# Kernel optimization log

Hardware: AMD Instinct MI355X
Metric: run time of the kernel (lower is better)

## Reference

```python
import jax, jax.numpy as jnp
import numpy as np

# Dims: T=64 steps, B=8 batch, H=128 hidden, NH=4 heads, D=2*H=256 cell dim
T, B, H, NH = 64, 8, 128, 4
D = 2 * H
EPS = 1e-5


def _bn(v, scale, bias):
    # flax BatchNorm (training mode): stats over all axes except feature (-1)
    axes = tuple(range(v.ndim - 1))
    mu = v.mean(axes, keepdims=True)
    var = v.var(axes, keepdims=True)
    return (v - mu) * jax.lax.rsqrt(var + EPS) * scale + bias


def setup_inputs() -> dict:
    key = jax.random.key(0)
    ks = iter(jax.random.split(key, 48))
    r = lambda shape, s=0.02: (jax.random.normal(next(ks), shape, jnp.float32) * s)
    z = lambda shape: jnp.zeros(shape, jnp.float32)
    o = lambda shape: jnp.ones(shape, jnp.float32)
    inp = {
        "x": jax.random.normal(next(ks), (T, B, H), jnp.float32),
        # per-head mLSTMCell params (stacked over NH heads), flax Linear: y = x @ W + b
        "Wq": r((NH, D, D)), "bq": z((NH, D)),
        "Wk": r((NH, D, D)), "bk": z((NH, D)),
        "Wv": r((NH, D, D)), "bv": z((NH, D)),
        "conv_k": r((4, 1, NH), 0.2), "conv_b": z((NH,)),  # 1->NH channel conv == per-head 1->1 conv
        "Wi": r((NH, D)), "bi": r((NH,), 0.01),
        "Wf": r((NH, D)),
        "bf": jax.random.uniform(next(ks), (NH,), jnp.float32, 3.0, 6.0),
        "Wo": r((NH, D, D)), "bo": z((NH, D)),
        "Wskip": r((NH, D, D)), "bskip": z((NH, D)),
        # block params
        "bn1_s": o((H,)), "bn1_b": z((H,)),
        "bn2_s": o((D,)), "bn2_b": z((D,)),
        "Wup1": r((H, D)), "bup1": z((D,)),
        "Wup2": r((H, D)), "bup2": z((D,)),
        "Wpoll": r((NH * D, D)), "bpoll": z((D,)),
        "Wdown": r((D, H)), "bdown": z((H,)),
    }
    return inp


def reference(x, Wq, bq, Wk, bk, Wv, bv, conv_k, conv_b, Wi, bi, Wf, bf,
              Wo, bo, Wskip, bskip, bn1_s, bn1_b, bn2_s, bn2_b,
              Wup1, bup1, Wup2, bup2, Wpoll, bpoll, Wdown, bdown):
    nh, d, _ = Wq.shape
    b = x.shape[1]
    inv_sqrt_d = 1.0 / jnp.sqrt(jnp.float32(d))

    def step(carry, xt):
        c, n, m = carry  # c: [nh,b,d,d], n: [nh,b,d], m: [nh,b]
        u = _bn(xt, bn1_s, bn1_b)                      # [b,H]
        trig = jax.nn.silu(u @ Wup2 + bup2)            # [b,d]
        xin = u @ Wup1 + bup1                          # [b,d] mlstm input
        outg = jax.nn.sigmoid(jnp.einsum('bd,hde->hbe', xin, Wo) + bo[:, None, :])
        it = jnp.einsum('bd,hd->hb', xin, Wi) + bi[:, None]
        ft = jnp.einsum('bd,hd->hb', xin, Wf) + bf[:, None]
        m_new = jnp.maximum(ft + m, it)
        ig = jnp.exp(it - m_new)
        fg = jnp.exp(ft + m - m_new)
        # causal-ish depthwise conv over feature axis (flax Conv SAME, k=4)
        qk = jax.lax.conv_general_dilated(xin[..., None], conv_k, (1,), 'SAME',
                                          dimension_numbers=('NWC', 'WIO', 'NWC')) + conv_b
        qk = jax.nn.silu(jnp.transpose(qk, (2, 0, 1)))  # [nh,b,d]
        k = (jnp.einsum('hbd,hde->hbe', qk, Wk) + bk[:, None, :]) * inv_sqrt_d
        q = jnp.einsum('hbd,hde->hbe', qk, Wq) + bq[:, None, :]
        v = jnp.einsum('bd,hde->hbe', xin, Wv) + bv[:, None, :]
        c_new = fg[:, :, None, None] * c + jnp.einsum('hb,hbi,hbj->hbij', ig, v, k)
        n_new = fg[..., None] * n + ig[..., None] * k
        scaler = 1.0 / jnp.maximum(jnp.abs(jnp.einsum('hbi,hbi->hb', n_new, q)), 1.0)
        h = outg * jnp.einsum('hbik,hbk->hbi', c_new, q) * scaler[..., None]
        h = h + jnp.einsum('hbd,hde->hbe', qk, Wskip) + bskip[:, None, :]
        ho = _bn(h, bn2_s, bn2_b)                      # [nh,b,d]
        ho = jnp.transpose(ho, (1, 0, 2)).reshape(b, nh * d)
        ho = ho @ Wpoll + bpoll                        # [b,d]
        y = (ho * trig) @ Wdown + bdown + xt           # residual
        return (c_new, n_new, m_new), y

    c0 = jnp.zeros((nh, b, d, d), x.dtype)
    n0 = jnp.zeros((nh, b, d), x.dtype)
    m0 = jnp.zeros((nh, b), x.dtype)
    _, ys = jax.lax.scan(step, (c0, n0, m0), x)
    return ys
```

## Files before the change

### kernel.cpp

```cpp
#include <hip/hip_runtime.h>
#include <hip/hip_bf16.h>

#define T_ 64
#define B_ 8
#define H_ 128
#define NH_ 4
#define D_ 256
#define TB_ 512
#define EPS_ 1e-5f

typedef short bf16x8 __attribute__((ext_vector_type(8)));
typedef float f32x4 __attribute__((ext_vector_type(4)));

__device__ __forceinline__ float silu_(float x){ return x / (1.0f + __expf(-x)); }
__device__ __forceinline__ float sigm_(float x){ return 1.0f / (1.0f + __expf(-x)); }
__device__ __forceinline__ unsigned short tobf_(float f){
  unsigned u = __float_as_uint(f);
  u += 0x7FFF + ((u >> 16) & 1);
  return (unsigned short)(u >> 16);
}
__device__ __forceinline__ int afrag_(int m, int k){
  return (((m >> 4)*8 + (k >> 5))*64 + ((k >> 3)&3)*16 + (m & 15))*8 + (k & 7);
}
__device__ __forceinline__ int afrag1024_(int m, int k){
  return (((m >> 4)*32 + (k >> 5))*64 + ((k >> 3)&3)*16 + (m & 15))*8 + (k & 7);
}

__device__ __forceinline__ void conv_tile_(const float* __restrict__ Win,
                                           unsigned short* __restrict__ Wout,
                                           int rowstride, int KBS, int tk, int tn,
                                           float (*tl)[132], int tid){
  #pragma unroll
  for (int p = 0; p < 2; p++){
    int r  = p*8 + (tid >> 5);
    int c4 = (tid & 31)*4;
    const float4 v = *(const float4*)(Win + (tk*16 + r)*rowstride + tn*128 + c4);
    tl[r][c4+0] = v.x; tl[r][c4+1] = v.y; tl[r][c4+2] = v.z; tl[r][c4+3] = v.w;
  }
  __syncthreads();
  int nn  = tid >> 5;
  int lqb = (tid >> 4) & 1;
  int lm  = tid & 15;
  int combo = (tn*8 + nn)*KBS + (tk >> 1);
  int l = (2*(tk & 1) + lqb)*16 + lm;
  bf16x8 v;
  #pragma unroll
  for (int j = 0; j < 8; j++) v[j] = (short)tobf_(tl[lqb*8 + j][nn*16 + lm]);
  *(bf16x8*)(Wout + (combo*64 + l)*8) = v;
}

__global__ __launch_bounds__(256) void k_prepup(
    const float* __restrict__ Wq, const float* __restrict__ Wk, const float* __restrict__ Ws,
    const float* __restrict__ Wv, const float* __restrict__ Wo,
    const float* __restrict__ Wup1, const float* __restrict__ Wup2,
    const float* __restrict__ Wp, const float* __restrict__ Wd,
    const float* __restrict__ x, const float* __restrict__ bn1s, const float* __restrict__ bn1b,
    const float* __restrict__ bup1, const float* __restrict__ bup2,
    const float* __restrict__ ck, const float* __restrict__ cb,
    const float* __restrict__ Wi, const float* __restrict__ bi,
    const float* __restrict__ Wf, const float* __restrict__ bfv,
    unsigned short* __restrict__ Wqt, unsigned short* __restrict__ Wkt,
    unsigned short* __restrict__ Wst, unsigned short* __restrict__ Wvt,
    unsigned short* __restrict__ Wot,
    unsigned short* __restrict__ Wpt, unsigned short* __restrict__ Wdt,
    unsigned short* __restrict__ xinb, unsigned short* __restrict__ qkb,
    float* __restrict__ trig, float* __restrict__ itb, float* __restrict__ ftb){
  __shared__ float xs[16][257];
  __shared__ unsigned short ubl[2048];
  __shared__ float tl[16][132];
  int bid = blockIdx.x;
  int tid = threadIdx.x;
  if (bid < 64){
    int u = bid;
    int mat = u >> 5, rt = u & 31;
    {
      int tt = tid >> 7, hf = tid & 127;
      int t = rt*2 + tt;
      const float* xp = x + t*(B_*H_) + hf;
      float v0[8]; float mu = 0.f;
      #pragma unroll
      for (int b = 0; b < 8; b++){ v0[b] = xp[b*H_]; mu += v0[b]; }
      mu *= 0.125f;
      float var = 0.f;
      #pragma unroll
      for (int b = 0; b < 8; b++){ float dd = v0[b]-mu; var += dd*dd; }
      var *= 0.125f;
      float sc = (1.0f/sqrtf(var + EPS_)) * bn1s[hf];
      float bs = bn1b[hf];
      int kb = hf >> 5, j = hf & 7;
      int lanebase = ((hf >> 3)&3)*16 + tt*8;
      unsigned short* up = ubl + kb*512 + j;
      #pragma unroll
      for (int b = 0; b < 8; b++)
        up[(lanebase + b)*8] = tobf_((v0[b]-mu)*sc + bs);
    }
    __syncthreads();
    int w = tid >> 6, l = tid & 63, lm = l & 15, lq = l >> 4;
    const float* Wf32 = (mat == 0) ? Wup1 : Wup2;
    f32x4 acc[4];
    #pragma unroll
    for (int nt = 0; nt < 4; nt++) acc[nt] = (f32x4){0.f,0.f,0.f,0.f};
    #pragma unroll
    for (int kb = 0; kb < 4; kb++){
      bf16x8 a = *(const bf16x8*)(ubl + kb*512 + l*8);
      int k0 = kb*32 + lq*8;
      #pragma unroll
      for (int nt = 0; nt < 4; nt++){
        int n = (w*4 + nt)*16 + lm;
        const float* src = Wf32 + k0*D_ + n;
        bf16x8 bfr;
        #pragma unroll
        for (int j = 0; j < 8; j++) bfr[j] = (short)tobf_(src[j*D_]);
        acc[nt] = __builtin_amdgcn_mfma_f32_16x16x32_bf16(a, bfr, acc[nt], 0, 0, 0);
      }
    }
    const float* bias = (mat == 0) ? bup1 : bup2;
    #pragma unroll
    for (int nt = 0; nt < 4; nt++){
      #pragma unroll
      for (int r = 0; r < 4; r++){
        int m = lq*4 + r;
        int row = rt*16 + m;
        int e = w*64 + nt*16 + lm;
        float vv = acc[nt][r] + bias[e];
        if (mat == 1){
          trig[row*D_ + e] = silu_(vv);
        } else {
          xs[m][e] = vv;
        }
      }
    }
    if (mat == 0){
      __syncthreads();
      int m = tid & 15;
      int oct2 = tid >> 4;
      int rowg = rt*16 + m;
      #pragma unroll
      for (int pass = 0; pass < 2; pass++){
        int d0 = (oct2 + pass*16) << 3;
        float xv[11];
        #pragma unroll
        for (int i = 0; i < 11; i++){
          int d = d0 - 1 + i;
          xv[i] = (d >= 0 && d <= 255) ? xs[m][d] : 0.f;
        }
        int fa = afrag_(rowg, d0);
        bf16x8 xo;
        #pragma unroll
        for (int j = 0; j < 8; j++) xo[j] = (short)tobf_(xv[j+1]);
        *(bf16x8*)(xinb + fa) = xo;
        #pragma unroll
        for (int h = 0; h < NH_; h++){
          float c0 = ck[0*NH_+h], c1 = ck[1*NH_+h], c2 = ck[2*NH_+h], c3 = ck[3*NH_+h];
          float cbh = cb[h];
          bf16x8 qv;
          #pragma unroll
          for (int j = 0; j < 8; j++){
            float a2 = cbh;
            a2 = fmaf(xv[j],   c0, a2);
            a2 = fmaf(xv[j+1], c1, a2);
            a2 = fmaf(xv[j+2], c2, a2);
            a2 = fmaf(xv[j+3], c3, a2);
            qv[j] = (short)tobf_(silu_(a2));
          }
          *(bf16x8*)(qkb + h*(TB_*D_) + fa) = qv;
        }
      }
      int dot = tid >> 2, l4 = tid & 3;
      int h = dot >> 4, mm = dot & 15;
      float ai = 0.f, af = 0.f;
      const float* wi = Wi + h*D_;
      const float* wf = Wf + h*D_;
      #pragma unroll 8
      for (int jj = 0; jj < 64; jj++){
        int k = l4*64 + jj;
        float xval = xs[mm][k];
        ai = fmaf(xval, wi[k], ai);
        af = fmaf(xval, wf[k], af);
      }
      ai += __shfl_down(ai, 1); af += __shfl_down(af, 1);
      ai += __shfl_down(ai, 2); af += __shfl_down(af, 2);
      if (l4 == 0){
        int rowg2 = rt*16 + mm;
        int t = rowg2 >> 3, b = rowg2 & 7;
        itb[(h*B_ + b)*T_ + t] = ai + bi[h];
        ftb[(h*B_ + b)*T_ + t] = af + bfv[h];
      }
    }
  } else if (bid < 704){
    int u = bid - 64;
    int sub = u & 31;
    int h   = (u >> 5) & 3;
    int mat = u >> 7;
    const float* Win; unsigned short* Wout;
    switch (mat){
      case 0: Win = Wq; Wout = Wqt; break;
      case 1: Win = Wk; Wout = Wkt; break;
      case 2: Win = Ws; Wout = Wst; break;
      case 3: Win = Wv; Wout = Wvt; break;
      default: Win = Wo; Wout = Wot; break;
    }
    conv_tile_(Win + h*(D_*D_), Wout + h*(D_*D_), D_, 8, sub & 15, sub >> 4, tl, tid);
  } else if (bid < 832){
    int u = bid - 704;
    conv_tile_(Wp, Wpt, D_, 32, u & 63, u >> 6, tl, tid);
  } else {
    int u = bid - 832;
    conv_tile_(Wd, Wdt, H_, 8, u, 0, tl, tid);
  }
}

__global__ __launch_bounds__(256) void k_gemm5(
    const unsigned short* __restrict__ qkb, const unsigned short* __restrict__ xinb,
    const unsigned short* __restrict__ Wqt, const unsigned short* __restrict__ Wkt,
    const unsigned short* __restrict__ Wst, const unsigned short* __restrict__ Wvt,
    const unsigned short* __restrict__ Wot,
    const float* __restrict__ bq, const float* __restrict__ bk, const float* __restrict__ bsk,
    const float* __restrict__ bv, const float* __restrict__ bo,
    unsigned short* __restrict__ qob, unsigned short* __restrict__ kob,
    unsigned short* __restrict__ vot,
    float* __restrict__ hb, float* __restrict__ og){
  int bid = blockIdx.x;
  int rt  = bid & 15;
  int h   = (bid >> 4) & 3;
  int mat = bid >> 6;
  int tid = threadIdx.x;
  int w = tid >> 6, l = tid & 63;
  int lm = l & 15, lq = l >> 4;
  int r0 = rt * 32;
  const unsigned short* A = (mat < 3) ? (qkb + h*(TB_*D_)) : xinb;
  const unsigned short* Bt;
  const float* bias;
  switch (mat){
    case 0: Bt = Wqt; bias = bq;  break;
    case 1: Bt = Wkt; bias = bk;  break;
    case 2: Bt = Wst; bias = bsk; break;
    case 3: Bt = Wvt; bias = bv;  break;
    default: Bt = Wot; bias = bo; break;
  }
  Bt += h*(D_*D_);
  f32x4 acc[2][4];
  #pragma unroll
  for (int mt = 0; mt < 2; mt++)
    #pragma unroll
    for (int nt = 0; nt < 4; nt++) acc[mt][nt] = (f32x4){0.f,0.f,0.f,0.f};
  const unsigned short* Ap = A + l*8;
  const unsigned short* Bp = Bt + l*8;
  #pragma unroll
  for (int kc = 0; kc < 8; kc++){
    bf16x8 a0 = *(const bf16x8*)(Ap + ((rt*16      + kc) << 9));
    bf16x8 a1 = *(const bf16x8*)(Ap + ((rt*16 + 8  + kc) << 9));
    bf16x8 b0 = *(const bf16x8*)(Bp + (((w*4+0)*8 + kc) << 9));
    bf16x8 b1 = *(const bf16x8*)(Bp + (((w*4+1)*8 + kc) << 9));
    bf16x8 b2 = *(const bf16x8*)(Bp + (((w*4+2)*8 + kc) << 9));
    bf16x8 b3 = *(const bf16x8*)(Bp + (((w*4+3)*8 + kc) << 9));
    acc[0][0] = __builtin_amdgcn_mfma_f32_16x16x32_bf16(a0, b0, acc[0][0], 0, 0, 0);
    acc[0][1] = __builtin_amdgcn_mfma_f32_16x16x32_bf16(a0, b1, acc[0][1], 0, 0, 0);
    acc[0][2] = __builtin_amdgcn_mfma_f32_16x16x32_bf16(a0, b2, acc[0][2], 0, 0, 0);
    acc[0][3] = __builtin_amdgcn_mfma_f32_16x16x32_bf16(a0, b3, acc[0][3], 0, 0, 0);
    acc[1][0] = __builtin_amdgcn_mfma_f32_16x16x32_bf16(a1, b0, acc[1][0], 0, 0, 0);
    acc[1][1] = __builtin_amdgcn_mfma_f32_16x16x32_bf16(a1, b1, acc[1][1], 0, 0, 0);
    acc[1][2] = __builtin_amdgcn_mfma_f32_16x16x32_bf16(a1, b2, acc[1][2], 0, 0, 0);
    acc[1][3] = __builtin_amdgcn_mfma_f32_16x16x32_bf16(a1, b3, acc[1][3], 0, 0, 0);
  }
  float bval[4];
  #pragma unroll
  for (int nt = 0; nt < 4; nt++) bval[nt] = bias[h*D_ + w*64 + nt*16 + lm];
  #pragma unroll
  for (int mt = 0; mt < 2; mt++){
    #pragma unroll
    for (int r = 0; r < 4; r++){
      int row = r0 + mt*16 + lq*4 + r;
      int t = row >> 3, b = row & 7;
      #pragma unroll
      for (int nt = 0; nt < 4; nt++){
        int e = w*64 + nt*16 + lm;
        float vv = acc[mt][nt][r] + bval[nt];
        if (mat <= 1){
          if (mat == 1) vv *= 0.0625f;
          unsigned short* ob = (mat == 0) ? qob : kob;
          int mt2 = t >> 4, kb2 = e >> 5;
          int lane2 = ((e >> 3)&3)*16 + (t & 15);
          ob[(h*B_ + b)*16384 + ((mt2*8 + kb2)*64 + lane2)*8 + (e & 7)] = tobf_(vv);
        } else if (mat == 3){
          int nt3 = e >> 4, kb3 = t >> 5;
          int lane3 = ((t >> 3)&3)*16 + lm;
          vot[(h*B_ + b)*16384 + ((nt3*2 + kb3)*64 + lane3)*8 + (t & 7)] = tobf_(vv);
        } else {
          int obase = (((t*NH_ + h)*B_ + b) << 8) + e;
          if (mat == 4) og[obase] = sigm_(vv);
          else          hb[obase] = vv;
        }
      }
    }
  }
}

__global__ __launch_bounds__(256) void k_attn2(
    const unsigned short* __restrict__ qob, const unsigned short* __restrict__ kob,
    const unsigned short* __restrict__ vot, const float* __restrict__ og,
    const float* __restrict__ itb, const float* __restrict__ ftb,
    float* __restrict__ hb){
  __shared__ unsigned short Pf[1024];
  __shared__ float partial[4][16];
  __shared__ float scal[16];
  int bid = blockIdx.x;
  int hbx = bid >> 2, tq = bid & 3;
  int h = hbx >> 3, b = hbx & 7;
  int tid = threadIdx.x;
  int w = tid >> 6, l = tid & 63, lm = l & 15, lq = l >> 4;
  float F  = ftb[hbx*T_ + l];
  float it = itb[hbx*T_ + l];
  #pragma unroll
  for (int off = 1; off < 64; off <<= 1){
    float v2 = __shfl_up(F, off);
    if (l >= off) F += v2;
  }
  float ct = it - F;
  float G = ct;
  #pragma unroll
  for (int off = 1; off < 64; off <<= 1){
    float v2 = __shfl_up(G, off);
    if (l >= off) G = fmaxf(G, v2);
  }
  float rb = -fmaxf(0.f, G);
  const unsigned short* Aq = qob + hbx*16384 + l*8;
  const unsigned short* Bk = kob + hbx*16384 + l*8;
  f32x4 accs = (f32x4){0.f,0.f,0.f,0.f};
  #pragma unroll
  for (int kc = 0; kc < 8; kc++){
    bf16x8 a  = *(const bf16x8*)(Aq + ((tq*8 + kc) << 9));
    bf16x8 bb = *(const bf16x8*)(Bk + ((w*8  + kc) << 9));
    accs = __builtin_amdgcn_mfma_f32_16x16x32_bf16(a, bb, accs, 0, 0, 0);
  }
  int s = w*16 + lm;
  float ct_s = __shfl(ct, s);
  float p[4], ps[4];
  #pragma unroll
  for (int r = 0; r < 4; r++){
    int t = tq*16 + lq*4 + r;
    float rb_t = __shfl(rb, t);
    float pv = (s <= t) ? __expf(ct_s + rb_t) * accs[r] : 0.f;
    p[r] = pv; ps[r] = pv;
  }
  #pragma unroll
  for (int off = 1; off < 16; off <<= 1){
    #pragma unroll
    for (int r = 0; r < 4; r++) ps[r] += __shfl_xor(ps[r], off);
  }
  if (lm == 0){
    #pragma unroll
    for (int r = 0; r < 4; r++) partial[w][lq*4 + r] = ps[r];
  }
  {
    int kbP = w >> 1;
    int laneP = ((w*2 + (lm >> 3)) & 3)*16;
    int jP = lm & 7;
    #pragma unroll
    for (int r = 0; r < 4; r++){
      int m = lq*4 + r;
      Pf[(kbP*64 + laneP + m)*8 + jP] = tobf_(p[r]);
    }
  }
  __syncthreads();
  if (tid < 16){
    float sum = partial[0][tid] + partial[1][tid] + partial[2][tid] + partial[3][tid];
    scal[tid] = 1.0f / fmaxf(fabsf(sum), 1.0f);
  }
  bf16x8 pa0 = *(const bf16x8*)(Pf + l*8);
  bf16x8 pa1 = *(const bf16x8*)(Pf + 512 + l*8);
  const unsigned short* Bv = vot + hbx*16384 + l*8;
  f32x4 acco[4];
  #pragma unroll
  for (int nt = 0; nt < 4; nt++) acco[nt] = (f32x4){0.f,0.f,0.f,0.f};
  #pragma unroll
  for (int nt = 0; nt < 4; nt++){
    int nt3 = w*4 + nt;
    bf16x8 b0 = *(const bf16x8*)(Bv + (((nt3*2 + 0)) << 9));
    bf16x8 b1 = *(const bf16x8*)(Bv + (((nt3*2 + 1)) << 9));
    acco[nt] = __builtin_amdgcn_mfma_f32_16x16x32_bf16(pa0, b0, acco[nt], 0, 0, 0);
    acco[nt] = __builtin_amdgcn_mfma_f32_16x16x32_bf16(pa1, b1, acco[nt], 0, 0, 0);
  }
  __syncthreads();
  #pragma unroll
  for (int nt = 0; nt < 4; nt++){
    #pragma unroll
    for (int r = 0; r < 4; r++){
      int tl = lq*4 + r;
      int t = tq*16 + tl;
      int e = (w*4 + nt)*16 + lm;
      int idx = (((t*NH_ + h)*B_ + b) << 8) + e;
      hb[idx] += og[idx] * acco[nt][r] * scal[tl];
    }
  }
}

__global__ __launch_bounds__(256) void k_tail3(
    const float* __restrict__ hbuf, const float* __restrict__ bn2s, const float* __restrict__ bn2b,
    const unsigned short* __restrict__ Wpt, const float* __restrict__ bp,
    const float* __restrict__ trig, const unsigned short* __restrict__ Wdt,
    const float* __restrict__ bd, const float* __restrict__ x, float* __restrict__ y){
  __shared__ unsigned short hfr[16384];
  __shared__ unsigned short zf[4096];
  int u = blockIdx.x;
  int tid = threadIdx.x;
  int w = tid >> 6, l = tid & 63, lm = l & 15, lq = l >> 4;
  #pragma unroll
  for (int s = 0; s < 2; s++){
    int pair = tid + (s << 8);
    int tt = pair >> 8;
    int d  = pair & 255;
    int t  = u*2 + tt;
    const float* hp = hbuf + (t*NH_*B_)*D_ + d;
    float v[32]; float mu = 0.f;
    #pragma unroll
    for (int i = 0; i < 32; i++){ v[i] = hp[i*D_]; mu += v[i]; }
    mu *= (1.0f/32.0f);
    float var = 0.f;
    #pragma unroll
    for (int i = 0; i < 32; i++){ float dd = v[i]-mu; var += dd*dd; }
    var *= (1.0f/32.0f);
    float sc = (1.0f/sqrtf(var + EPS_)) * bn2s[d];
    float bs = bn2b[d];
    #pragma unroll
    for (int i = 0; i < 32; i++){
      int hh = i >> 3, b = i & 7;
      int m = tt*8 + b;
      int k = hh*D_ + d;
      hfr[afrag1024_(m, k)] = tobf_((v[i]-mu)*sc + bs);
    }
  }
  __syncthreads();
  f32x4 acc[4];
  #pragma unroll
  for (int nt = 0; nt < 4; nt++) acc[nt] = (f32x4){0.f,0.f,0.f,0.f};
  const unsigned short* Apl = hfr + l*8;
  const unsigned short* Bp  = Wpt + l*8;
  #pragma unroll 4
  for (int kc = 0; kc < 32; kc++){
    bf16x8 a = *(const bf16x8*)(Apl + (kc << 9));
    #pragma unroll
    for (int nt = 0; nt < 4; nt++){
      bf16x8 bfr = *(const bf16x8*)(Bp + ((((w*4+nt)*32) + kc) << 9));
      acc[nt] = __builtin_amdgcn_mfma_f32_16x16x32_bf16(a, bfr, acc[nt], 0, 0, 0);
    }
  }
  #pragma unroll
  for (int nt = 0; nt < 4; nt++){
    int e = w*64 + nt*16 + lm;
    float bpe = bp[e];
    #pragma unroll
    for (int r = 0; r < 4; r++){
      int ml = lq*4 + r;
      int row = u*16 + ml;
      float z = (acc[nt][r] + bpe) * trig[row*D_ + e];
      zf[afrag_(ml, e)] = tobf_(z);
    }
  }
  __syncthreads();
  f32x4 acc2[2];
  acc2[0] = (f32x4){0.f,0.f,0.f,0.f};
  acc2[1] = (f32x4){0.f,0.f,0.f,0.f};
  const unsigned short* Bdp = Wdt + l*8;
  #pragma unroll
  for (int kc = 0; kc < 8; kc++){
    bf16x8 a = *(const bf16x8*)(zf + (kc << 9) + l*8);
    #pragma unroll
    for (int q = 0; q < 2; q++){
      bf16x8 bb = *(const bf16x8*)(Bdp + (((w*2+q)*8 + kc) << 9));
      acc2[q] = __builtin_amdgcn_mfma_f32_16x16x32_bf16(a, bb, acc2[q], 0, 0, 0);
    }
  }
  #pragma unroll
  for (int q = 0; q < 2; q++){
    int hh = (w*2+q)*16 + lm;
    float bde = bd[hh];
    #pragma unroll
    for (int r = 0; r < 4; r++){
      int row = u*16 + lq*4 + r;
      y[row*H_ + hh] = acc2[q][r] + bde + x[row*H_ + hh];
    }
  }
}

extern "C" void kernel_launch(void* const* d_in, const int* in_sizes, int n_in,
                              void* d_out, int out_size, void* d_ws, size_t ws_size,
                              hipStream_t stream){
  const float* x     = (const float*)d_in[0];
  const float* Wq    = (const float*)d_in[1];
  const float* bq    = (const float*)d_in[2];
  const float* Wk    = (const float*)d_in[3];
  const float* bk    = (const float*)d_in[4];
  const float* Wv    = (const float*)d_in[5];
  const float* bv    = (const float*)d_in[6];
  const float* ck    = (const float*)d_in[7];
  const float* cb    = (const float*)d_in[8];
  const float* Wi    = (const float*)d_in[9];
  const float* bi    = (const float*)d_in[10];
  const float* Wf    = (const float*)d_in[11];
  const float* bf    = (const float*)d_in[12];
  const float* Wo    = (const float*)d_in[13];
  const float* bo    = (const float*)d_in[14];
  const float* Wsk   = (const float*)d_in[15];
  const float* bsk   = (const float*)d_in[16];
  const float* bn1s  = (const float*)d_in[17];
  const float* bn1b  = (const float*)d_in[18];
  const float* bn2s  = (const float*)d_in[19];
  const float* bn2b  = (const float*)d_in[20];
  const float* Wup1  = (const float*)d_in[21];
  const float* bup1  = (const float*)d_in[22];
  const float* Wup2  = (const float*)d_in[23];
  const float* bup2  = (const float*)d_in[24];
  const float* Wp    = (const float*)d_in[25];
  const float* bp    = (const float*)d_in[26];
  const float* Wd    = (const float*)d_in[27];
  const float* bd    = (const float*)d_in[28];
  float* y = (float*)d_out;

  float* w = (float*)d_ws;
  float* trig = w;  w += T_*B_*D_;
  float* hbuf = w;  w += T_*NH_*B_*D_;
  float* og   = w;  w += T_*NH_*B_*D_;
  float* itb  = w;  w += NH_*B_*T_;
  float* ftb  = w;  w += NH_*B_*T_;
  unsigned short* xinb = (unsigned short*)w;  w += (T_*B_*D_)/2;
  unsigned short* qkb  = (unsigned short*)w;  w += (NH_*TB_*D_)/2;
  unsigned short* Wqt  = (unsigned short*)w;  w += (NH_*D_*D_)/2;
  unsigned short* Wkt  = (unsigned short*)w;  w += (NH_*D_*D_)/2;
  unsigned short* Wst  = (unsigned short*)w;  w += (NH_*D_*D_)/2;
  unsigned short* Wvt  = (unsigned short*)w;  w += (NH_*D_*D_)/2;
  unsigned short* Wot  = (unsigned short*)w;  w += (NH_*D_*D_)/2;
  unsigned short* qob  = (unsigned short*)w;  w += (NH_*B_*T_*D_)/2;
  unsigned short* kob  = (unsigned short*)w;  w += (NH_*B_*T_*D_)/2;
  unsigned short* vot  = (unsigned short*)w;  w += (NH_*B_*T_*D_)/2;
  unsigned short* Wpt  = (unsigned short*)w;  w += (NH_*D_*D_)/2;
  unsigned short* Wdt  = (unsigned short*)w;  w += (D_*H_)/2;

  k_prepup<<<848, 256, 0, stream>>>(Wq, Wk, Wsk, Wv, Wo, Wup1, Wup2, Wp, Wd,
                                    x, bn1s, bn1b, bup1, bup2, ck, cb, Wi, bi, Wf, bf,
                                    Wqt, Wkt, Wst, Wvt, Wot, Wpt, Wdt,
                                    xinb, qkb, trig, itb, ftb);
  k_gemm5<<<320, 256, 0, stream>>>(qkb, xinb, Wqt, Wkt, Wst, Wvt, Wot,
                                   bq, bk, bsk, bv, bo, qob, kob, vot, hbuf, og);
  k_attn2<<<NH_*B_*4, 256, 0, stream>>>(qob, kob, vot, og, itb, ftb, hbuf);
  k_tail3<<<32, 256, 0, stream>>>(hbuf, bn2s, bn2b, Wpt, bp, trig, Wdt, bd, x, y);
}
```

Before: 151.7 us.

## Fuse projection GEMMs and attention into one per-(head,batch) kernel

Merges the five projection GEMMs (q, k, skip, v, output gate) and the chunked attention step into a single kernel with one block per head-batch pair. Each block computes all 64 timesteps of every projection, writes them to global memory, synchronises, then loops over the four query chunks for the attention. This removes one kernel launch and the inter-kernel dependency. In exchange it cuts the grid from several hundred blocks to 32 and serialises far more MFMA work and weight loads inside each block, so occupancy and latency hiding drop.

```diff
diff --git a/kernel.cpp b/kernel.cpp
--- a/kernel.cpp
+++ b/kernel.cpp
@@ -210,102 +210,21 @@
   }
 }
 
-__global__ __launch_bounds__(256) void k_gemm5(
+__global__ __launch_bounds__(256) void k_fuse(
     const unsigned short* __restrict__ qkb, const unsigned short* __restrict__ xinb,
     const unsigned short* __restrict__ Wqt, const unsigned short* __restrict__ Wkt,
     const unsigned short* __restrict__ Wst, const unsigned short* __restrict__ Wvt,
     const unsigned short* __restrict__ Wot,
     const float* __restrict__ bq, const float* __restrict__ bk, const float* __restrict__ bsk,
     const float* __restrict__ bv, const float* __restrict__ bo,
+    const float* __restrict__ itb, const float* __restrict__ ftb,
     unsigned short* __restrict__ qob, unsigned short* __restrict__ kob,
     unsigned short* __restrict__ vot,
     float* __restrict__ hb, float* __restrict__ og){
-  int bid = blockIdx.x;
-  int rt  = bid & 15;
-  int h   = (bid >> 4) & 3;
-  int mat = bid >> 6;
-  int tid = threadIdx.x;
-  int w = tid >> 6, l = tid & 63;
-  int lm = l & 15, lq = l >> 4;
-  int r0 = rt * 32;
-  const unsigned short* A = (mat < 3) ? (qkb + h*(TB_*D_)) : xinb;
-  const unsigned short* Bt;
-  const float* bias;
-  switch (mat){
-    case 0: Bt = Wqt; bias = bq;  break;
-    case 1: Bt = Wkt; bias = bk;  break;
-    case 2: Bt = Wst; bias = bsk; break;
-    case 3: Bt = Wvt; bias = bv;  break;
-    default: Bt = Wot; bias = bo; break;
-  }
-  Bt += h*(D_*D_);
-  f32x4 acc[2][4];
-  #pragma unroll
-  for (int mt = 0; mt < 2; mt++)
-    #pragma unroll
-    for (int nt = 0; nt < 4; nt++) acc[mt][nt] = (f32x4){0.f,0.f,0.f,0.f};
-  const unsigned short* Ap = A + l*8;
-  const unsigned short* Bp = Bt + l*8;
-  #pragma unroll
-  for (int kc = 0; kc < 8; kc++){
-    bf16x8 a0 = *(const bf16x8*)(Ap + ((rt*16      + kc) << 9));
-    bf16x8 a1 = *(const bf16x8*)(Ap + ((rt*16 + 8  + kc) << 9));
-    bf16x8 b0 = *(const bf16x8*)(Bp + (((w*4+0)*8 + kc) << 9));
-    bf16x8 b1 = *(const bf16x8*)(Bp + (((w*4+1)*8 + kc) << 9));
-    bf16x8 b2 = *(const bf16x8*)(Bp + (((w*4+2)*8 + kc) << 9));
-    bf16x8 b3 = *(const bf16x8*)(Bp + (((w*4+3)*8 + kc) << 9));
-    acc[0][0] = __builtin_amdgcn_mfma_f32_16x16x32_bf16(a0, b0, acc[0][0], 0, 0, 0);
-    acc[0][1] = __builtin_amdgcn_mfma_f32_16x16x32_bf16(a0, b1, acc[0][1], 0, 0, 0);
-    acc[0][2] = __builtin_amdgcn_mfma_f32_16x16x32_bf16(a0, b2, acc[0][2], 0, 0, 0);
-    acc[0][3] = __builtin_amdgcn_mfma_f32_16x16x32_bf16(a0, b3, acc[0][3], 0, 0, 0);
-    acc[1][0] = __builtin_amdgcn_mfma_f32_16x16x32_bf16(a1, b0, acc[1][0], 0, 0, 0);
-    acc[1][1] = __builtin_amdgcn_mfma_f32_16x16x32_bf16(a1, b1, acc[1][1], 0, 0, 0);
-    acc[1][2] = __builtin_amdgcn_mfma_f32_16x16x32_bf16(a1, b2, acc[1][2], 0, 0, 0);
-    acc[1][3] = __builtin_amdgcn_mfma_f32_16x16x32_bf16(a1, b3, acc[1][3], 0, 0, 0);
-  }
-  float bval[4];
-  #pragma unroll
-  for (int nt = 0; nt < 4; nt++) bval[nt] = bias[h*D_ + w*64 + nt*16 + lm];
-  #pragma unroll
-  for (int mt = 0; mt < 2; mt++){
-    #pragma unroll
-    for (int r = 0; r < 4; r++){
-      int row = r0 + mt*16 + lq*4 + r;
-      int t = row >> 3, b = row & 7;
-      #pragma unroll
-      for (int nt = 0; nt < 4; nt++){
-        int e = w*64 + nt*16 + lm;
-        float vv = acc[mt][nt][r] + bval[nt];
-        if (mat <= 1){
-          if (mat == 1) vv *= 0.0625f;
-          unsigned short* ob = (mat == 0) ? qob : kob;
-          int mt2 = t >> 4, kb2 = e >> 5;
-          int lane2 = ((e >> 3)&3)*16 + (t & 15);
-          ob[(h*B_ + b)*16384 + ((mt2*8 + kb2)*64 + lane2)*8 + (e & 7)] = tobf_(vv);
-        } else if (mat == 3){
-          int nt3 = e >> 4, kb3 = t >> 5;
-          int lane3 = ((t >> 3)&3)*16 + lm;
-          vot[(h*B_ + b)*16384 + ((nt3*2 + kb3)*64 + lane3)*8 + (t & 7)] = tobf_(vv);
-        } else {
-          int obase = (((t*NH_ + h)*B_ + b) << 8) + e;
-          if (mat == 4) og[obase] = sigm_(vv);
-          else          hb[obase] = vv;
-        }
-      }
-    }
-  }
-}
-
-__global__ __launch_bounds__(256) void k_attn2(
-    const unsigned short* __restrict__ qob, const unsigned short* __restrict__ kob,
-    const unsigned short* __restrict__ vot, const float* __restrict__ og,
-    const float* __restrict__ itb, const float* __restrict__ ftb,
-    float* __restrict__ hb){
   __shared__ unsigned short Pf[1024];
   __shared__ float partial[4][16];
   __shared__ float scal[16];
-  int bid = blockIdx.x;
-  int hbx = bid >> 2, tq = bid & 3;
+  int hbx = blockIdx.x;
   int h = hbx >> 3, b = hbx & 7;
   int tid = threadIdx.x;
   int w = tid >> 6, l = tid & 63, lm = l & 15, lq = l >> 4;
@@ -324,73 +243,141 @@
     if (l >= off) G = fmaxf(G, v2);
   }
   float rb = -fmaxf(0.f, G);
+  for (int mat = 0; mat < 5; mat++){
+    const unsigned short* A = (mat < 3) ? (qkb + h*(TB_*D_)) : xinb;
+    const unsigned short* Bt;
+    const float* bias;
+    switch (mat){
+      case 0: Bt = Wqt; bias = bq;  break;
+      case 1: Bt = Wkt; bias = bk;  break;
+      case 2: Bt = Wst; bias = bsk; break;
+      case 3: Bt = Wvt; bias = bv;  break;
+      default: Bt = Wot; bias = bo; break;
+    }
+    Bt += h*(D_*D_);
+    f32x4 acc[4][4];
+    #pragma unroll
+    for (int mt = 0; mt < 4; mt++)
+      #pragma unroll
+      for (int nt = 0; nt < 4; nt++) acc[mt][nt] = (f32x4){0.f,0.f,0.f,0.f};
+    const unsigned short* Bp = Bt + l*8;
+    #pragma unroll
+    for (int kc = 0; kc < 8; kc++){
+      bf16x8 a[4];
+      #pragma unroll
+      for (int mt = 0; mt < 4; mt++){
+        int row = (mt*16 + lm)*8 + b;
+        a[mt] = *(const bf16x8*)(A + (((row >> 4)*8 + kc)*64 + lq*16 + (row & 15))*8);
+      }
+      #pragma unroll
+      for (int nt = 0; nt < 4; nt++){
+        bf16x8 bb = *(const bf16x8*)(Bp + (((w*4+nt)*8 + kc) << 9));
+        #pragma unroll
+        for (int mt = 0; mt < 4; mt++)
+          acc[mt][nt] = __builtin_amdgcn_mfma_f32_16x16x32_bf16(a[mt], bb, acc[mt][nt], 0, 0, 0);
+      }
+    }
+    float bval[4];
+    #pragma unroll
+    for (int nt = 0; nt < 4; nt++) bval[nt] = bias[h*D_ + w*64 + nt*16 + lm];
+    #pragma unroll
+    for (int mt = 0; mt < 4; mt++){
+      #pragma unroll
+      for (int r = 0; r < 4; r++){
+        int t = mt*16 + lq*4 + r;
+        #pragma unroll
+        for (int nt = 0; nt < 4; nt++){
+          int e = w*64 + nt*16 + lm;
+          float vv = acc[mt][nt][r] + bval[nt];
+          if (mat <= 1){
+            if (mat == 1) vv *= 0.0625f;
+            unsigned short* ob = (mat == 0) ? qob : kob;
+            int kb2 = e >> 5;
+            int lane2 = ((e >> 3)&3)*16 + (t & 15);
+            ob[hbx*16384 + (((t >> 4)*8 + kb2)*64 + lane2)*8 + (e & 7)] = tobf_(vv);
+          } else if (mat == 3){
+            int nt3 = e >> 4, kb3 = t >> 5;
+            int lane3 = ((t >> 3)&3)*16 + lm;
+            vot[hbx*16384 + ((nt3*2 + kb3)*64 + lane3)*8 + (t & 7)] = tobf_(vv);
+          } else {
+            int obase = (((t*NH_ + h)*B_ + b) << 8) + e;
+            if (mat == 4) og[obase] = sigm_(vv);
+            else          hb[obase] = vv;
+          }
+        }
+      }
+    }
+  }
+  __syncthreads();
   const unsigned short* Aq = qob + hbx*16384 + l*8;
   const unsigned short* Bk = kob + hbx*16384 + l*8;
-  f32x4 accs = (f32x4){0.f,0.f,0.f,0.f};
-  #pragma unroll
-  for (int kc = 0; kc < 8; kc++){
-    bf16x8 a  = *(const bf16x8*)(Aq + ((tq*8 + kc) << 9));
-    bf16x8 bb = *(const bf16x8*)(Bk + ((w*8  + kc) << 9));
-    accs = __builtin_amdgcn_mfma_f32_16x16x32_bf16(a, bb, accs, 0, 0, 0);
-  }
-  int s = w*16 + lm;
-  float ct_s = __shfl(ct, s);
-  float p[4], ps[4];
-  #pragma unroll
-  for (int r = 0; r < 4; r++){
-    int t = tq*16 + lq*4 + r;
-    float rb_t = __shfl(rb, t);
-    float pv = (s <= t) ? __expf(ct_s + rb_t) * accs[r] : 0.f;
-    p[r] = pv; ps[r] = pv;
-  }
-  #pragma unroll
-  for (int off = 1; off < 16; off <<= 1){
-    #pragma unroll
-    for (int r = 0; r < 4; r++) ps[r] += __shfl_xor(ps[r], off);
-  }
-  if (lm == 0){
-    #pragma unroll
-    for (int r = 0; r < 4; r++) partial[w][lq*4 + r] = ps[r];
-  }
-  {
-    int kbP = w >> 1;
-    int laneP = ((w*2 + (lm >> 3)) & 3)*16;
-    int jP = lm & 7;
+  const unsigned short* Bv = vot + hbx*16384 + l*8;
+  for (int tq = 0; tq < 4; tq++){
+    f32x4 accs = (f32x4){0.f,0.f,0.f,0.f};
+    #pragma unroll
+    for (int kc = 0; kc < 8; kc++){
+      bf16x8 a  = *(const bf16x8*)(Aq + ((tq*8 + kc) << 9));
+      bf16x8 bb = *(const bf16x8*)(Bk + ((w*8  + kc) << 9));
+      accs = __builtin_amdgcn_mfma_f32_16x16x32_bf16(a, bb, accs, 0, 0, 0);
+    }
+    int s = w*16 + lm;
+    float ct_s = __shfl(ct, s);
+    float p[4], ps[4];
     #pragma unroll
     for (int r = 0; r < 4; r++){
-      int m = lq*4 + r;
-      Pf[(kbP*64 + laneP + m)*8 + jP] = tobf_(p[r]);
-    }
-  }
-  __syncthreads();
-  if (tid < 16){
-    float sum = partial[0][tid] + partial[1][tid] + partial[2][tid] + partial[3][tid];
-    scal[tid] = 1.0f / fmaxf(fabsf(sum), 1.0f);
-  }
-  bf16x8 pa0 = *(const bf16x8*)(Pf + l*8);
-  bf16x8 pa1 = *(const bf16x8*)(Pf + 512 + l*8);
-  const unsigned short* Bv = vot + hbx*16384 + l*8;
-  f32x4 acco[4];
-  #pragma unroll
-  for (int nt = 0; nt < 4; nt++) acco[nt] = (f32x4){0.f,0.f,0.f,0.f};
-  #pragma unroll
-  for (int nt = 0; nt < 4; nt++){
-    int nt3 = w*4 + nt;
-    bf16x8 b0 = *(const bf16x8*)(Bv + (((nt3*2 + 0)) << 9));
-    bf16x8 b1 = *(const bf16x8*)(Bv + (((nt3*2 + 1)) << 9));
-    acco[nt] = __builtin_amdgcn_mfma_f32_16x16x32_bf16(pa0, b0, acco[nt], 0, 0, 0);
-    acco[nt] = __builtin_amdgcn_mfma_f32_16x16x32_bf16(pa1, b1, acco[nt], 0, 0, 0);
-  }
-  __syncthreads();
-  #pragma unroll
-  for (int nt = 0; nt < 4; nt++){
-    #pragma unroll
-    for (int r = 0; r < 4; r++){
-      int tl = lq*4 + r;
-      int t = tq*16 + tl;
-      int e = (w*4 + nt)*16 + lm;
-      int idx = (((t*NH_ + h)*B_ + b) << 8) + e;
-      hb[idx] += og[idx] * acco[nt][r] * scal[tl];
+      int t = tq*16 + lq*4 + r;
+      float rb_t = __shfl(rb, t);
+      float pv = (s <= t) ? __expf(ct_s + rb_t) * accs[r] : 0.f;
+      p[r] = pv; ps[r] = pv;
+    }
+    #pragma unroll
+    for (int off = 1; off < 16; off <<= 1){
+      #pragma unroll
+      for (int r = 0; r < 4; r++) ps[r] += __shfl_xor(ps[r], off);
+    }
+    if (lm == 0){
+      #pragma unroll
+      for (int r = 0; r < 4; r++) partial[w][lq*4 + r] = ps[r];
+    }
+    {
+      int kbP = w >> 1;
+      int laneP = ((w*2 + (lm >> 3)) & 3)*16;
+      int jP = lm & 7;
+      #pragma unroll
+      for (int r = 0; r < 4; r++){
+        int m = lq*4 + r;
+        Pf[(kbP*64 + laneP + m)*8 + jP] = tobf_(p[r]);
+      }
+    }
+    __syncthreads();
+    if (tid < 16){
+      float sum = partial[0][tid] + partial[1][tid] + partial[2][tid] + partial[3][tid];
+      scal[tid] = 1.0f / fmaxf(fabsf(sum), 1.0f);
+    }
+    bf16x8 pa0 = *(const bf16x8*)(Pf + l*8);
+    bf16x8 pa1 = *(const bf16x8*)(Pf + 512 + l*8);
+    f32x4 acco[4];
+    #pragma unroll
+    for (int nt = 0; nt < 4; nt++) acco[nt] = (f32x4){0.f,0.f,0.f,0.f};
+    #pragma unroll
+    for (int nt = 0; nt < 4; nt++){
+      int nt3 = w*4 + nt;
+      bf16x8 b0 = *(const bf16x8*)(Bv + (((nt3*2 + 0)) << 9));
+      bf16x8 b1 = *(const bf16x8*)(Bv + (((nt3*2 + 1)) << 9));
+      acco[nt] = __builtin_amdgcn_mfma_f32_16x16x32_bf16(pa0, b0, acco[nt], 0, 0, 0);
+      acco[nt] = __builtin_amdgcn_mfma_f32_16x16x32_bf16(pa1, b1, acco[nt], 0, 0, 0);
+    }
+    __syncthreads();
+    #pragma unroll
+    for (int nt = 0; nt < 4; nt++){
+      #pragma unroll
+      for (int r = 0; r < 4; r++){
+        int tl = lq*4 + r;
+        int t = tq*16 + tl;
+        int e = (w*4 + nt)*16 + lm;
+        int idx = (((t*NH_ + h)*B_ + b) << 8) + e;
+        hb[idx] += og[idx] * acco[nt][r] * scal[tl];
+      }
     }
   }
 }
@@ -540,8 +527,8 @@
                                     x, bn1s, bn1b, bup1, bup2, ck, cb, Wi, bi, Wf, bf,
                                     Wqt, Wkt, Wst, Wvt, Wot, Wpt, Wdt,
                                     xinb, qkb, trig, itb, ftb);
-  k_gemm5<<<320, 256, 0, stream>>>(qkb, xinb, Wqt, Wkt, Wst, Wvt, Wot,
-                                   bq, bk, bsk, bv, bo, qob, kob, vot, hbuf, og);
-  k_attn2<<<NH_*B_*4, 256, 0, stream>>>(qob, kob, vot, og, itb, ftb, hbuf);
+  k_fuse<<<NH_*B_, 256, 0, stream>>>(qkb, xinb, Wqt, Wkt, Wst, Wvt, Wot,
+                                     bq, bk, bsk, bv, bo, itb, ftb,
+                                     qob, kob, vot, hbuf, og);
   k_tail3<<<32, 256, 0, stream>>>(hbuf, bn2s, bn2b, Wpt, bp, trig, Wdt, bd, x, y);
 }
```

Result: slower. 241.1 us (+58.9%).
